# Optimization experiments

Measured on AMD Instinct MI355X. Metric: run time of the kernel, lower is better.

## Reference

```python
import jax, jax.numpy as jnp
import numpy as np

EPS = 1e-5

def _mlp(x, W1, b1, W2, b2):
    h = jax.nn.gelu(x @ W1 + b1, approximate=False)
    return h @ W2 + b2

def _ln(x, g, b):
    m = jnp.mean(x, axis=-1, keepdims=True)
    v = jnp.mean((x - m) ** 2, axis=-1, keepdims=True)
    return (x - m) * jax.lax.rsqrt(v + EPS) * g + b

def setup_inputs() -> dict:
    key = jax.random.key(0)
    B, N, D = 4, 256, 128
    ks = jax.random.split(key, 32)
    s = 0.02
    inp = {
        "node_h": jax.random.normal(ks[0], (B, N, D), jnp.float32),
        "pair_h": jax.random.normal(ks[1], (B, N, N, D), jnp.float32),
        "node_mask": jax.random.randint(ks[2], (B, N), 0, 2, jnp.int32),
        "edge_mask": jax.random.randint(ks[3], (B, N, N), 0, 2, jnp.int32),
        # node_from_pair MLP: 3D -> 2D -> D
        "nfp_W1": jax.random.normal(ks[4], (3 * D, 2 * D), jnp.float32) * s,
        "nfp_b1": jnp.zeros((2 * D,), jnp.float32),
        "nfp_W2": jax.random.normal(ks[5], (2 * D, D), jnp.float32) * s,
        "nfp_b2": jnp.zeros((D,), jnp.float32),
        # pair_from_node MLP: 5D -> 2D -> D
        "pfn_W1": jax.random.normal(ks[6], (5 * D, 2 * D), jnp.float32) * s,
        "pfn_b1": jnp.zeros((2 * D,), jnp.float32),
        "pfn_W2": jax.random.normal(ks[7], (2 * D, D), jnp.float32) * s,
        "pfn_b2": jnp.zeros((D,), jnp.float32),
        # node_ff: D -> 4D -> D
        "nff_W1": jax.random.normal(ks[8], (D, 4 * D), jnp.float32) * s,
        "nff_b1": jnp.zeros((4 * D,), jnp.float32),
        "nff_W2": jax.random.normal(ks[9], (4 * D, D), jnp.float32) * s,
        "nff_b2": jnp.zeros((D,), jnp.float32),
        # pair_ff: D -> 4D -> D
        "pff_W1": jax.random.normal(ks[10], (D, 4 * D), jnp.float32) * s,
        "pff_b1": jnp.zeros((4 * D,), jnp.float32),
        "pff_W2": jax.random.normal(ks[11], (4 * D, D), jnp.float32) * s,
        "pff_b2": jnp.zeros((D,), jnp.float32),
        # gates: 2D -> D, sigmoid
        "og_W": jax.random.normal(ks[12], (2 * D, D), jnp.float32) * s,
        "og_b": jnp.zeros((D,), jnp.float32),
        "ig_W": jax.random.normal(ks[13], (2 * D, D), jnp.float32) * s,
        "ig_b": jnp.zeros((D,), jnp.float32),
        # LayerNorms
        "nn1_g": jnp.ones((D,), jnp.float32), "nn1_b": jnp.zeros((D,), jnp.float32),
        "nn2_g": jnp.ones((D,), jnp.float32), "nn2_b": jnp.zeros((D,), jnp.float32),
        "pn1_g": jnp.ones((D,), jnp.float32), "pn1_b": jnp.zeros((D,), jnp.float32),
        "pn2_g": jnp.ones((D,), jnp.float32), "pn2_b": jnp.zeros((D,), jnp.float32),
    }
    return inp

def reference(node_h, pair_h, node_mask, edge_mask,
              nfp_W1, nfp_b1, nfp_W2, nfp_b2,
              pfn_W1, pfn_b1, pfn_W2, pfn_b2,
              nff_W1, nff_b1, nff_W2, nff_b2,
              pff_W1, pff_b1, pff_W2, pff_b2,
              og_W, og_b, ig_W, ig_b,
              nn1_g, nn1_b, nn2_g, nn2_b,
              pn1_g, pn1_b, pn2_g, pn2_b):
    vp = edge_mask.astype(jnp.float32)                       # [B,N,N]
    pair_m = pair_h * vp[..., None]                          # masked pairs
    out_deg = jnp.clip(vp.sum(axis=2), 1.0)[..., None]       # [B,N,1]
    in_deg = jnp.clip(vp.sum(axis=1), 1.0)[..., None]        # [B,N,1]
    out_ctx_raw = pair_m.sum(axis=2) / out_deg               # [B,N,D]
    in_ctx_raw = pair_m.sum(axis=1) / in_deg                 # [B,N,D]
    out_g = jax.nn.sigmoid(jnp.concatenate([node_h, out_ctx_raw], -1) @ og_W + og_b)
    in_g = jax.nn.sigmoid(jnp.concatenate([node_h, in_ctx_raw], -1) @ ig_W + ig_b)
    node_upd = _mlp(jnp.concatenate([node_h, out_g * out_ctx_raw, in_g * in_ctx_raw], -1),
                    nfp_W1, nfp_b1, nfp_W2, nfp_b2)
    node_h = _ln(node_h + node_upd, nn1_g, nn1_b)
    node_h = _ln(node_h + _mlp(node_h, nff_W1, nff_b1, nff_W2, nff_b2), nn2_g, nn2_b)
    node_h = node_h * node_mask.astype(jnp.float32)[..., None]

    B, N, D = node_h.shape
    hi = jnp.broadcast_to(node_h[:, :, None, :], (B, N, N, D))
    hj = jnp.broadcast_to(node_h[:, None, :, :], (B, N, N, D))
    feat = jnp.concatenate([pair_h, hi, hj, hi - hj, hi * hj], -1)  # [B,N,N,5D]
    pair_upd = _mlp(feat, pfn_W1, pfn_b1, pfn_W2, pfn_b2)
    pair_h = _ln(pair_h + pair_upd, pn1_g, pn1_b)
    pair_h = _ln(pair_h + _mlp(pair_h, pff_W1, pff_b1, pff_W2, pff_b2), pn2_g, pn2_b)
    pair_h = pair_h * vp[..., None]
    return (node_h, pair_h)
```

## Files before the change

kernel.cpp:

```cpp
#include <hip/hip_runtime.h>
#include <hip/hip_bf16.h>

#define DI __device__ __forceinline__

typedef float f32x4 __attribute__((ext_vector_type(4)));
typedef float f32x2 __attribute__((ext_vector_type(2)));
typedef short s16x8 __attribute__((ext_vector_type(8)));
typedef short s16x4 __attribute__((ext_vector_type(4)));
typedef unsigned u32x2 __attribute__((ext_vector_type(2)));
typedef unsigned u32x4 __attribute__((ext_vector_type(4)));

DI short f2bf(float x) {
  union { float f; unsigned u; } v; v.f = x;
  unsigned r = v.u + 0x7fffu + ((v.u >> 16) & 1u);
  return (short)(r >> 16);
}

DI float bf2f(short x) {
  union { unsigned u; float f; } v;
  v.u = ((unsigned)(unsigned short)x) << 16;
  return v.f;
}

DI unsigned cvt_pk(float lo, float hi) {
  unsigned r;
  asm("v_cvt_pk_bf16_f32 %0, %1, %2" : "=v"(r) : "v"(lo), "v"(hi));
  return r;
}

DI s16x8 pack8(f32x4 a, f32x4 b) {
  union { u32x4 u; s16x8 s; } r;
  r.u[0] = cvt_pk(a[0], a[1]); r.u[1] = cvt_pk(a[2], a[3]);
  r.u[2] = cvt_pk(b[0], b[1]); r.u[3] = cvt_pk(b[2], b[3]);
  return r.s;
}

DI float gelu_f(float x) {
  const float e = __expf(-x * fmaf(x * x, 0.0713548162f, 1.5957691216f));
  return __fdividef(x, 1.f + e);
}

__global__ __launch_bounds__(256) void prep_ctx_kernel(
    const float* __restrict__ pair_h, const int* __restrict__ edge_mask,
    const float* __restrict__ pfnW1, const float* __restrict__ pfnW2,
    const float* __restrict__ pffW1, const float* __restrict__ pffW2,
    short* __restrict__ W1c, float* __restrict__ Wu, float* __restrict__ Whjv,
    short* __restrict__ W2T, short* __restrict__ W1Tp,
    short* __restrict__ W2Tp, float* __restrict__ out_ctx,
    float* __restrict__ in_ctx) {
  __shared__ float sacc[2][128];
  __shared__ float sdeg[2];
  const int t = threadIdx.x;
  if (blockIdx.x >= 2048) {
    int idx = (blockIdx.x - 2048) * 256 + t;
    if (idx < 65536) {
      int n = idx / 256, k = idx % 256;
      float v = (k < 128) ? pfnW1[k * 256 + n] : pfnW1[(384 + k) * 256 + n];
      W1c[idx] = f2bf(v);
      return;
    }
    idx -= 65536;
    if (idx < 32768) {
      int k = idx / 256, n = idx % 256;
      Wu[idx] = pfnW1[(128 + k) * 256 + n] + pfnW1[(384 + k) * 256 + n];
      return;
    }
    idx -= 32768;
    if (idx < 32768) {
      int k = idx / 256, n = idx % 256;
      Whjv[idx] = pfnW1[(256 + k) * 256 + n] - pfnW1[(384 + k) * 256 + n];
      return;
    }
    idx -= 32768;
    if (idx < 32768) {
      int n = idx / 256, k = idx % 256;
      W2T[idx] = f2bf(pfnW2[k * 128 + n]);
      return;
    }
    idx -= 32768;
    if (idx < 65536) {
      int n = idx / 128, k = idx % 128;
      W1Tp[idx] = f2bf(pffW1[k * 512 + n]);
      return;
    }
    idx -= 65536;
    if (idx < 65536) {
      int n = idx / 512, k = idx % 512;
      W2Tp[idx] = f2bf(pffW2[k * 128 + n]);
    }
    return;
  }
  const int wg = blockIdx.x;
  const int half = t >> 7, d = t & 127;
  const bool outmode = wg < 1024;
  const int w2 = outmode ? wg : wg - 1024;
  const int b = w2 >> 8, x = w2 & 255;
  float acc = 0.f, deg = 0.f;
#pragma unroll 8
  for (int y0 = 0; y0 < 256; y0 += 2) {
    const int y = y0 + half;
    int row;
    if (outmode) row = (b * 256 + x) * 256 + y;
    else row = (b * 256 + y) * 256 + x;
    const float m = (float)edge_mask[row];
    const float v = pair_h[(long)row * 128 + d];
    acc = fmaf(m, v, acc);
    deg += m;
  }
  sacc[half][d] = acc;
  if (d == 0) sdeg[half] = deg;
  __syncthreads();
  if (t < 128) {
    float tot = sacc[0][d] + sacc[1][d];
    float dg = fmaxf(sdeg[0] + sdeg[1], 1.f);
    float* dst = outmode ? out_ctx : in_ctx;
    dst[(b * 256 + x) * 128 + d] = tot / dg;
  }
}

__global__ __launch_bounds__(256) void node_kernel(
    const float* __restrict__ node_h, const float* __restrict__ out_ctx,
    const float* __restrict__ in_ctx, const int* __restrict__ node_mask,
    const float* __restrict__ ogW, const float* __restrict__ ogb,
    const float* __restrict__ igW, const float* __restrict__ igb,
    const float* __restrict__ nW1, const float* __restrict__ nb1,
    const float* __restrict__ nW2, const float* __restrict__ nb2,
    const float* __restrict__ fW1, const float* __restrict__ fb1,
    const float* __restrict__ fW2, const float* __restrict__ fb2,
    const float* __restrict__ g1, const float* __restrict__ be1,
    const float* __restrict__ g2, const float* __restrict__ be2,
    const float* __restrict__ Wu, const float* __restrict__ ub1,
    const float* __restrict__ Whjv, float* __restrict__ out_node,
    short* __restrict__ node_bf, short* __restrict__ u_bf,
    short* __restrict__ hjv_bf) {
  __shared__ float sh[4][896];
  __shared__ float fin[4][128];
  const int t = threadIdx.x;
  const int wv = t >> 6, lane = t & 63;
  float* const xn = sh[wv];
  float* const xo = sh[wv] + 128;
  float* const xi = sh[wv] + 256;
  float* const hh = sh[wv] + 384;
  const int row = blockIdx.x * 4 + wv;

#pragma unroll
  for (int c = 0; c < 2; ++c) {
    const int col = lane + 64 * c;
    xn[col] = node_h[row * 128 + col];
    xo[col] = out_ctx[row * 128 + col];
    xi[col] = in_ctx[row * 128 + col];
  }

  {
    float ao[2], ai[2];
#pragma unroll
    for (int c = 0; c < 2; ++c) {
      const int col = lane + 64 * c;
      ao[c] = ogb[col];
      ai[c] = igb[col];
    }
#pragma unroll 4
    for (int k = 0; k < 256; ++k) {
      float xov, xiv;
      if (k < 128) { xov = xiv = xn[k]; }
      else { xov = xo[k - 128]; xiv = xi[k - 128]; }
#pragma unroll
      for (int c = 0; c < 2; ++c) {
        const int col = lane + 64 * c;
        ao[c] += xov * ogW[k * 128 + col];
        ai[c] += xiv * igW[k * 128 + col];
      }
    }
#pragma unroll
    for (int c = 0; c < 2; ++c) {
      const int col = lane + 64 * c;
      const float go = 1.f / (1.f + __expf(-ao[c]));
      const float gi = 1.f / (1.f + __expf(-ai[c]));
      xo[col] *= go;
      xi[col] *= gi;
    }
  }

  {
    float a1[4];
#pragma unroll
    for (int c = 0; c < 4; ++c) a1[c] = nb1[lane + 64 * c];
#pragma unroll 4
    for (int k = 0; k < 384; ++k) {
      const float* src = (k < 128) ? xn : (k < 256) ? xo : xi;
      const float x = src[k & 127];
#pragma unroll
      for (int c = 0; c < 4; ++c) a1[c] += x * nW1[k * 256 + lane + 64 * c];
    }
#pragma unroll
    for (int c = 0; c < 4; ++c) hh[lane + 64 * c] = gelu_f(a1[c]);
  }
  {
    float a2[2];
#pragma unroll
    for (int c = 0; c < 2; ++c) a2[c] = nb2[lane + 64 * c];
#pragma unroll 4
    for (int k = 0; k < 256; ++k) {
      const float h = hh[k];
#pragma unroll
      for (int c = 0; c < 2; ++c) a2[c] += h * nW2[k * 128 + lane + 64 * c];
    }
    float v0 = xn[lane] + a2[0];
    float v1 = xn[lane + 64] + a2[1];
    float s = v0 + v1, ss = v0 * v0 + v1 * v1;
#pragma unroll
    for (int off = 1; off < 64; off <<= 1) {
      s += __shfl_xor(s, off, 64);
      ss += __shfl_xor(ss, off, 64);
    }
    const float m = s * (1.f / 128.f);
    const float var = ss * (1.f / 128.f) - m * m;
    const float rs = rsqrtf(var + 1e-5f);
    xn[lane] = (v0 - m) * rs * g1[lane] + be1[lane];
    xn[lane + 64] = (v1 - m) * rs * g1[lane + 64] + be1[lane + 64];
  }

  {
    float af[8];
#pragma unroll
    for (int c = 0; c < 8; ++c) af[c] = fb1[lane + 64 * c];
#pragma unroll 4
    for (int k = 0; k < 128; ++k) {
      const float x = xn[k];
#pragma unroll
      for (int c = 0; c < 8; ++c) af[c] += x * fW1[k * 512 + lane + 64 * c];
    }
#pragma unroll
    for (int c = 0; c < 8; ++c) hh[lane + 64 * c] = gelu_f(af[c]);
  }
  {
    float a2[2];
#pragma unroll
    for (int c = 0; c < 2; ++c) a2[c] = fb2[lane + 64 * c];
#pragma unroll 4
    for (int k = 0; k < 512; ++k) {
      const float h = hh[k];
#pragma unroll
      for (int c = 0; c < 2; ++c) a2[c] += h * fW2[k * 128 + lane + 64 * c];
    }
    float v0 = xn[lane] + a2[0];
    float v1 = xn[lane + 64] + a2[1];
    float s = v0 + v1, ss = v0 * v0 + v1 * v1;
#pragma unroll
    for (int off = 1; off < 64; off <<= 1) {
      s += __shfl_xor(s, off, 64);
      ss += __shfl_xor(ss, off, 64);
    }
    const float m = s * (1.f / 128.f);
    const float var = ss * (1.f / 128.f) - m * m;
    const float rs = rsqrtf(var + 1e-5f);
    const float msk = (float)node_mask[row];
    const float o0 = ((v0 - m) * rs * g2[lane] + be2[lane]) * msk;
    const float o1 = ((v1 - m) * rs * g2[lane + 64] + be2[lane + 64]) * msk;
    out_node[row * 128 + lane] = o0;
    out_node[row * 128 + lane + 64] = o1;
    node_bf[row * 128 + lane] = f2bf(o0);
    node_bf[row * 128 + lane + 64] = f2bf(o1);
    fin[wv][lane] = o0;
    fin[wv][lane + 64] = o1;
  }
  __syncthreads();
  {
    float uacc[4], hacc[4];
    const float bb = ub1[t];
#pragma unroll
    for (int r = 0; r < 4; ++r) { uacc[r] = bb; hacc[r] = 0.f; }
#pragma unroll 4
    for (int k = 0; k < 128; ++k) {
      const float wu = Wu[k * 256 + t];
      const float wh = Whjv[k * 256 + t];
#pragma unroll
      for (int r = 0; r < 4; ++r) {
        uacc[r] += fin[r][k] * wu;
        hacc[r] += fin[r][k] * wh;
      }
    }
#pragma unroll
    for (int r = 0; r < 4; ++r) {
      u_bf[(blockIdx.x * 4 + r) * 256 + t] = f2bf(uacc[r]);
      hjv_bf[(blockIdx.x * 4 + r) * 256 + t] = f2bf(hacc[r]);
    }
  }
}

__global__ __launch_bounds__(512, 4) void pair_kernel(
    const float* __restrict__ pair_h, const short* __restrict__ node_bf,
    const int* __restrict__ edge_mask, const short* __restrict__ W1c,
    const short* __restrict__ W2T, const short* __restrict__ W1Tp,
    const short* __restrict__ W2Tp, const short* __restrict__ u_bf,
    const short* __restrict__ hjv_bf, const float* __restrict__ b2,
    const float* __restrict__ b1p, const float* __restrict__ b2p,
    const float* __restrict__ g1, const float* __restrict__ be1,
    const float* __restrict__ g2, const float* __restrict__ be2,
    float* __restrict__ out_pair) {
  constexpr int OFF_A = 0, OFF_H1 = 0, OFF_Y = 0, OFF_H2 = 33792,
                OFF_SCR = 67584;
  constexpr int PA = 528, PY = 272;
  __shared__ __align__(16) char smem[69632];

  const int t = threadIdx.x;
  const int wg = blockIdx.x;
  const int b = wg >> 10, rem = wg & 1023;
  const int i = rem >> 2, j0 = (rem & 3) << 6;
  const int bi = (b << 8) + i;
  const long rowbase = (long)bi * 256 + j0;

  const int lane = t & 63, wv = t >> 6;
  const int lr = lane & 15, lq = lane >> 4;
  const int jb = (wv >> 2) * 32, nb2 = (wv & 3) * 32;

  {
    const int r = t >> 3, oc = t & 7, c0 = oc * 16;
    const float* prow = pair_h + (rowbase + r) * 128 + c0;
    const short* hjrow = node_bf + (b * 256 + j0 + r) * 128 + c0;
    const short* hirow = node_bf + (b * 256 + i) * 128 + c0;
    char* arow = smem + OFF_A + r * PA;
#pragma unroll
    for (int h = 0; h < 2; ++h) {
      f32x4 p0 = *(const f32x4*)(prow + h * 8);
      f32x4 p1 = *(const f32x4*)(prow + h * 8 + 4);
      s16x8 hj = *(const s16x8*)(hjrow + h * 8);
      s16x8 hi = *(const s16x8*)(hirow + h * 8);
      *(s16x8*)(arow + c0 * 2 + h * 16) = pack8(p0, p1);
      union { u32x4 u; s16x8 s; } pd;
#pragma unroll
      for (int e = 0; e < 4; ++e)
        pd.u[e] = cvt_pk(bf2f(hi[2 * e]) * bf2f(hj[2 * e]),
                         bf2f(hi[2 * e + 1]) * bf2f(hj[2 * e + 1]));
      *(s16x8*)(arow + 256 + c0 * 2 + h * 16) = pd.s;
    }
  }
  __syncthreads();

  f32x4 acc1[4][2];
#pragma unroll
  for (int jt = 0; jt < 4; ++jt)
#pragma unroll
    for (int nt = 0; nt < 2; ++nt) acc1[jt][nt] = {0.f, 0.f, 0.f, 0.f};
  {
    const int nb = wv * 32;
    const short* wp0 = W1c + (nb + lr) * 256 + lq * 8;
    const short* wp1 = W1c + (nb + 16 + lr) * 256 + lq * 8;
    s16x8 w0p[4], w1p[4];
#pragma unroll
    for (int pf = 0; pf < 4; ++pf) {
      w0p[pf] = *(const s16x8*)(wp0 + pf * 32);
      w1p[pf] = *(const s16x8*)(wp1 + pf * 32);
    }
    s16x8 dc[2][4];
#pragma unroll
    for (int pf = 0; pf < 2; ++pf)
#pragma unroll
      for (int jt = 0; jt < 4; ++jt)
        dc[pf][jt] = *(const s16x8*)(smem + OFF_A + (jt * 16 + lr) * PA +
                                     pf * 64 + lq * 16);
#pragma unroll
    for (int ks = 0; ks < 8; ++ks) {
      const int cur = ks & 1;
      s16x8 w0 = w0p[ks & 3], w1 = w1p[ks & 3];
      if (ks < 4) {
        w0p[ks & 3] = *(const s16x8*)(wp0 + (ks + 4) * 32);
        w1p[ks & 3] = *(const s16x8*)(wp1 + (ks + 4) * 32);
      }
      s16x8 d[4];
#pragma unroll
      for (int jt = 0; jt < 4; ++jt) d[jt] = dc[cur][jt];
      if (ks < 6) {
#pragma unroll
        for (int jt = 0; jt < 4; ++jt)
          dc[cur][jt] = *(const s16x8*)(smem + OFF_A + (jt * 16 + lr) * PA +
                                        (ks + 2) * 64 + lq * 16);
      }
#pragma unroll
      for (int jt = 0; jt < 4; ++jt) {
        acc1[jt][0] = __builtin_amdgcn_mfma_f32_16x16x32_bf16(w0, d[jt], acc1[jt][0], 0, 0, 0);
        acc1[jt][1] = __builtin_amdgcn_mfma_f32_16x16x32_bf16(w1, d[jt], acc1[jt][1], 0, 0, 0);
      }
    }
  }
  s16x4 uv0 = *(const s16x4*)(u_bf + bi * 256 + wv * 32 + lq * 4);
  s16x4 uv1 = *(const s16x4*)(u_bf + bi * 256 + wv * 32 + 16 + lq * 4);
  const short* q2p0 = W2T + (nb2 + lr) * 256 + lq * 8;
  const short* q2p1 = W2T + (nb2 + 16 + lr) * 256 + lq * 8;
  s16x8 q2w0[4], q2w1[4];
  q2w0[0] = *(const s16x8*)q2p0;
  q2w1[0] = *(const s16x8*)q2p1;
  q2w0[1] = *(const s16x8*)(q2p0 + 32);
  q2w1[1] = *(const s16x8*)(q2p1 + 32);
  __syncthreads();
  {
    const int nb = wv * 32;
#pragma unroll
    for (int nt = 0; nt < 2; ++nt) {
      const int n0 = nb + nt * 16 + lq * 4;
      const s16x4 uv = nt ? uv1 : uv0;
      f32x4 uu;
#pragma unroll
      for (int v = 0; v < 4; ++v) uu[v] = bf2f(uv[v]);
#pragma unroll
      for (int jt = 0; jt < 4; ++jt) {
        const int j = jt * 16 + lr;
        s16x4 hv = *(const s16x4*)(hjv_bf + (b * 256 + j0 + j) * 256 + n0);
        float pre[4];
#pragma unroll
        for (int v = 0; v < 4; ++v)
          pre[v] = acc1[jt][nt][v] + uu[v] + bf2f(hv[v]);
        u32x2 pk = {cvt_pk(gelu_f(pre[0]), gelu_f(pre[1])),
                    cvt_pk(gelu_f(pre[2]), gelu_f(pre[3]))};
        *(u32x2*)(smem + OFF_H1 + j * PA + n0 * 2) = pk;
      }
    }
  }
  __syncthreads();

  f32x4 x1v[2][2];
  {
    q2w0[2] = *(const s16x8*)(q2p0 + 64);
    q2w1[2] = *(const s16x8*)(q2p1 + 64);
    q2w0[3] = *(const s16x8*)(q2p0 + 96);
    q2w1[3] = *(const s16x8*)(q2p1 + 96);
    f32x4 pr[2][2];
#pragma unroll
    for (int nt = 0; nt < 2; ++nt)
#pragma unroll
      for (int jt = 0; jt < 2; ++jt)
        pr[jt][nt] = *(const f32x4*)(pair_h + (rowbase + jb + jt * 16 + lr) * 128 +
                                     nb2 + nt * 16 + lq * 4);
    s16x8 dc[2][2];
#pragma unroll
    for (int pf = 0; pf < 2; ++pf)
#pragma unroll
      for (int jt = 0; jt < 2; ++jt)
        dc[pf][jt] = *(const s16x8*)(smem + OFF_H1 + (jb + jt * 16 + lr) * PA +
                                     pf * 64 + lq * 16);
    f32x4 acc2[2][2];
#pragma unroll
    for (int jt = 0; jt < 2; ++jt)
#pragma unroll
      for (int nt = 0; nt < 2; ++nt) acc2[jt][nt] = {0.f, 0.f, 0.f, 0.f};
#pragma unroll
    for (int ks = 0; ks < 8; ++ks) {
      const int cur = ks & 1;
      s16x8 w0 = q2w0[ks & 3], w1 = q2w1[ks & 3];
      if (ks < 4) {
        q2w0[ks & 3] = *(const s16x8*)(q2p0 + (ks + 4) * 32);
        q2w1[ks & 3] = *(const s16x8*)(q2p1 + (ks + 4) * 32);
      }
      s16x8 d[2];
#pragma unroll
      for (int jt = 0; jt < 2; ++jt) d[jt] = dc[cur][jt];
      if (ks < 6) {
#pragma unroll
        for (int jt = 0; jt < 2; ++jt)
          dc[cur][jt] = *(const s16x8*)(smem + OFF_H1 + (jb + jt * 16 + lr) * PA +
                                        (ks + 2) * 64 + lq * 16);
      }
#pragma unroll
      for (int jt = 0; jt < 2; ++jt) {
        acc2[jt][0] = __builtin_amdgcn_mfma_f32_16x16x32_bf16(w0, d[jt], acc2[jt][0], 0, 0, 0);
        acc2[jt][1] = __builtin_amdgcn_mfma_f32_16x16x32_bf16(w1, d[jt], acc2[jt][1], 0, 0, 0);
      }
    }
#pragma unroll
    for (int nt = 0; nt < 2; ++nt) {
      const int n0 = nb2 + nt * 16 + lq * 4;
      f32x4 bv = *(const f32x4*)(b2 + n0);
#pragma unroll
      for (int jt = 0; jt < 2; ++jt)
        x1v[jt][nt] = acc2[jt][nt] + bv + pr[jt][nt];
    }
  }
  {
    float s[2], ss[2];
#pragma unroll
    for (int jt = 0; jt < 2; ++jt) {
      s[jt] = 0.f; ss[jt] = 0.f;
#pragma unroll
      for (int nt = 0; nt < 2; ++nt)
#pragma unroll
        for (int v = 0; v < 4; ++v) {
          const float x = x1v[jt][nt][v];
          s[jt] += x; ss[jt] += x * x;
        }
      s[jt] += __shfl_xor(s[jt], 16, 64);
      ss[jt] += __shfl_xor(ss[jt], 16, 64);
      s[jt] += __shfl_xor(s[jt], 32, 64);
      ss[jt] += __shfl_xor(ss[jt], 32, 64);
    }
    if (lq == 0) {
#pragma unroll
      for (int jt = 0; jt < 2; ++jt) {
        const int j = jb + jt * 16 + lr;
        f32x2 p = {s[jt], ss[jt]};
        *(f32x2*)(smem + OFF_SCR + j * 32 + (wv & 3) * 8) = p;
      }
    }
    __syncthreads();
    float lnm[2], lnr[2];
#pragma unroll
    for (int jt = 0; jt < 2; ++jt) {
      const int j = jb + jt * 16 + lr;
      f32x4 pA = *(const f32x4*)(smem + OFF_SCR + j * 32);
      f32x4 pB = *(const f32x4*)(smem + OFF_SCR + j * 32 + 16);
      const float S = pA[0] + pA[2] + pB[0] + pB[2];
      const float SS = pA[1] + pA[3] + pB[1] + pB[3];
      const float m = S * (1.f / 128.f);
      const float var = SS * (1.f / 128.f) - m * m;
      lnm[jt] = m;
      lnr[jt] = rsqrtf(var + 1e-5f);
    }
#pragma unroll
    for (int nt = 0; nt < 2; ++nt) {
      const int n0 = nb2 + nt * 16 + lq * 4;
      f32x4 gv = *(const f32x4*)(g1 + n0);
      f32x4 bv = *(const f32x4*)(be1 + n0);
#pragma unroll
      for (int jt = 0; jt < 2; ++jt) {
        const int j = jb + jt * 16 + lr;
        float y[4];
#pragma unroll
        for (int v = 0; v < 4; ++v)
          y[v] = (x1v[jt][nt][v] - lnm[jt]) * lnr[jt] * gv[v] + bv[v];
        u32x2 pk = {cvt_pk(y[0], y[1]), cvt_pk(y[2], y[3])};
        *(u32x2*)(smem + OFF_Y + j * PY + n0 * 2) = pk;
      }
    }
  }
  const short* g3p0a = W1Tp + (wv * 32 + lr) * 128 + lq * 8;
  const short* g3p1a = W1Tp + (wv * 32 + 16 + lr) * 128 + lq * 8;
  s16x8 g3w0[4], g3w1[4];
  g3w0[0] = *(const s16x8*)g3p0a;
  g3w1[0] = *(const s16x8*)g3p1a;
  g3w0[1] = *(const s16x8*)(g3p0a + 32);
  g3w1[1] = *(const s16x8*)(g3p1a + 32);
  const int em0 = edge_mask[rowbase + jb + lr];
  const int em1 = edge_mask[rowbase + jb + 16 + lr];
  __syncthreads();

  f32x4 acc4[2][2];
#pragma unroll
  for (int jt = 0; jt < 2; ++jt)
#pragma unroll
    for (int nt = 0; nt < 2; ++nt) acc4[jt][nt] = {0.f, 0.f, 0.f, 0.f};

#pragma unroll
  for (int p = 0; p < 2; ++p) {
    f32x4 acc3[4][2];
#pragma unroll
    for (int jt = 0; jt < 4; ++jt)
#pragma unroll
      for (int nt = 0; nt < 2; ++nt) acc3[jt][nt] = {0.f, 0.f, 0.f, 0.f};
    {
      const int nb3 = p * 256 + wv * 32;
      const short* wp0 = W1Tp + (nb3 + lr) * 128 + lq * 8;
      const short* wp1 = W1Tp + (nb3 + 16 + lr) * 128 + lq * 8;
      if (p == 0) {
        g3w0[2] = *(const s16x8*)(wp0 + 64);
        g3w1[2] = *(const s16x8*)(wp1 + 64);
        g3w0[3] = *(const s16x8*)(wp0 + 96);
        g3w1[3] = *(const s16x8*)(wp1 + 96);
      } else {
#pragma unroll
        for (int pf = 0; pf < 4; ++pf) {
          g3w0[pf] = *(const s16x8*)(wp0 + pf * 32);
          g3w1[pf] = *(const s16x8*)(wp1 + pf * 32);
        }
      }
#pragma unroll
      for (int ks = 0; ks < 4; ++ks) {
        s16x8 d[4];
#pragma unroll
        for (int jt = 0; jt < 4; ++jt)
          d[jt] = *(const s16x8*)(smem + OFF_Y + (jt * 16 + lr) * PY +
                                  ks * 64 + lq * 16);
#pragma unroll
        for (int jt = 0; jt < 4; ++jt) {
          acc3[jt][0] = __builtin_amdgcn_mfma_f32_16x16x32_bf16(g3w0[ks], d[jt], acc3[jt][0], 0, 0, 0);
          acc3[jt][1] = __builtin_amdgcn_mfma_f32_16x16x32_bf16(g3w1[ks], d[jt], acc3[jt][1], 0, 0, 0);
        }
      }
    }
    const short* qp0 = W2Tp + (nb2 + lr) * 512 + p * 256 + lq * 8;
    const short* qp1 = W2Tp + (nb2 + 16 + lr) * 512 + p * 256 + lq * 8;
    s16x8 q4w0[4], q4w1[4];
    q4w0[0] = *(const s16x8*)qp0;
    q4w1[0] = *(const s16x8*)qp1;
    q4w0[1] = *(const s16x8*)(qp0 + 32);
    q4w1[1] = *(const s16x8*)(qp1 + 32);
    if (p == 1) __syncthreads();
    {
#pragma unroll
      for (int nt = 0; nt < 2; ++nt) {
        const int n0l = wv * 32 + nt * 16 + lq * 4;
        f32x4 bv = *(const f32x4*)(b1p + p * 256 + n0l);
#pragma unroll
        for (int jt = 0; jt < 4; ++jt) {
          const int j = jt * 16 + lr;
          u32x2 pk = {cvt_pk(gelu_f(acc3[jt][nt][0] + bv[0]),
                             gelu_f(acc3[jt][nt][1] + bv[1])),
                      cvt_pk(gelu_f(acc3[jt][nt][2] + bv[2]),
                             gelu_f(acc3[jt][nt][3] + bv[3]))};
          *(u32x2*)(smem + OFF_H2 + j * PA + n0l * 2) = pk;
        }
      }
    }
    __syncthreads();
    {
      q4w0[2] = *(const s16x8*)(qp0 + 64);
      q4w1[2] = *(const s16x8*)(qp1 + 64);
      q4w0[3] = *(const s16x8*)(qp0 + 96);
      q4w1[3] = *(const s16x8*)(qp1 + 96);
      s16x8 dc[2][2];
#pragma unroll
      for (int pf = 0; pf < 2; ++pf)
#pragma unroll
        for (int jt = 0; jt < 2; ++jt)
          dc[pf][jt] = *(const s16x8*)(smem + OFF_H2 + (jb + jt * 16 + lr) * PA +
                                       pf * 64 + lq * 16);
#pragma unroll
      for (int ks = 0; ks < 8; ++ks) {
        const int cur = ks & 1;
        s16x8 w0 = q4w0[ks & 3], w1 = q4w1[ks & 3];
        if (ks < 4) {
          q4w0[ks & 3] = *(const s16x8*)(qp0 + (ks + 4) * 32);
          q4w1[ks & 3] = *(const s16x8*)(qp1 + (ks + 4) * 32);
        }
        s16x8 d[2];
#pragma unroll
        for (int jt = 0; jt < 2; ++jt) d[jt] = dc[cur][jt];
        if (ks < 6) {
#pragma unroll
          for (int jt = 0; jt < 2; ++jt)
            dc[cur][jt] = *(const s16x8*)(smem + OFF_H2 + (jb + jt * 16 + lr) * PA +
                                          (ks + 2) * 64 + lq * 16);
        }
#pragma unroll
        for (int jt = 0; jt < 2; ++jt) {
          acc4[jt][0] = __builtin_amdgcn_mfma_f32_16x16x32_bf16(w0, d[jt], acc4[jt][0], 0, 0, 0);
          acc4[jt][1] = __builtin_amdgcn_mfma_f32_16x16x32_bf16(w1, d[jt], acc4[jt][1], 0, 0, 0);
        }
      }
    }
  }

  f32x4 x2v[2][2];
#pragma unroll
  for (int nt = 0; nt < 2; ++nt) {
    const int n0 = nb2 + nt * 16 + lq * 4;
    f32x4 bv = *(const f32x4*)(b2p + n0);
#pragma unroll
    for (int jt = 0; jt < 2; ++jt) {
      const int j = jb + jt * 16 + lr;
      s16x4 yv = *(const s16x4*)(smem + OFF_Y + j * PY + n0 * 2);
      f32x4 yr;
#pragma unroll
      for (int v = 0; v < 4; ++v) yr[v] = bf2f(yv[v]);
      x2v[jt][nt] = acc4[jt][nt] + bv + yr;
    }
  }
  {
    float s[2], ss[2];
#pragma unroll
    for (int jt = 0; jt < 2; ++jt) {
      s[jt] = 0.f; ss[jt] = 0.f;
#pragma unroll
      for (int nt = 0; nt < 2; ++nt)
#pragma unroll
        for (int v = 0; v < 4; ++v) {
          const float x = x2v[jt][nt][v];
          s[jt] += x; ss[jt] += x * x;
        }
      s[jt] += __shfl_xor(s[jt], 16, 64);
      ss[jt] += __shfl_xor(ss[jt], 16, 64);
      s[jt] += __shfl_xor(s[jt], 32, 64);
      ss[jt] += __shfl_xor(ss[jt], 32, 64);
    }
    if (lq == 0) {
#pragma unroll
      for (int jt = 0; jt < 2; ++jt) {
        const int j = jb + jt * 16 + lr;
        f32x2 p = {s[jt], ss[jt]};
        *(f32x2*)(smem + OFF_SCR + j * 32 + (wv & 3) * 8) = p;
      }
    }
    __syncthreads();
    float lnm[2], lnr[2], vp[2];
#pragma unroll
    for (int jt = 0; jt < 2; ++jt) {
      const int j = jb + jt * 16 + lr;
      f32x4 pA = *(const f32x4*)(smem + OFF_SCR + j * 32);
      f32x4 pB = *(const f32x4*)(smem + OFF_SCR + j * 32 + 16);
      const float S = pA[0] + pA[2] + pB[0] + pB[2];
      const float SS = pA[1] + pA[3] + pB[1] + pB[3];
      const float m = S * (1.f / 128.f);
      const float var = SS * (1.f / 128.f) - m * m;
      lnm[jt] = m;
      lnr[jt] = rsqrtf(var + 1e-5f);
      vp[jt] = (float)(jt ? em1 : em0);
    }
#pragma unroll
    for (int nt = 0; nt < 2; ++nt) {
      const int n0 = nb2 + nt * 16 + lq * 4;
      f32x4 gv = *(const f32x4*)(g2 + n0);
      f32x4 bv = *(const f32x4*)(be2 + n0);
#pragma unroll
      for (int jt = 0; jt < 2; ++jt) {
        const int j = jb + jt * 16 + lr;
        f32x4 o;
#pragma unroll
        for (int v = 0; v < 4; ++v)
          o[v] = ((x2v[jt][nt][v] - lnm[jt]) * lnr[jt] * gv[v] + bv[v]) * vp[jt];
        *(f32x4*)(out_pair + (rowbase + j) * 128 + n0) = o;
      }
    }
  }
}

extern "C" void kernel_launch(void* const* d_in, const int* in_sizes, int n_in,
                              void* d_out, int out_size, void* d_ws,
                              size_t ws_size, hipStream_t stream) {
  const float* node_h = (const float*)d_in[0];
  const float* pair_h = (const float*)d_in[1];
  const int* node_mask = (const int*)d_in[2];
  const int* edge_mask = (const int*)d_in[3];
  const float* nfp_W1 = (const float*)d_in[4];
  const float* nfp_b1 = (const float*)d_in[5];
  const float* nfp_W2 = (const float*)d_in[6];
  const float* nfp_b2 = (const float*)d_in[7];
  const float* pfn_W1 = (const float*)d_in[8];
  const float* pfn_b1 = (const float*)d_in[9];
  const float* pfn_W2 = (const float*)d_in[10];
  const float* pfn_b2 = (const float*)d_in[11];
  const float* nff_W1 = (const float*)d_in[12];
  const float* nff_b1 = (const float*)d_in[13];
  const float* nff_W2 = (const float*)d_in[14];
  const float* nff_b2 = (const float*)d_in[15];
  const float* pff_W1 = (const float*)d_in[16];
  const float* pff_b1 = (const float*)d_in[17];
  const float* pff_W2 = (const float*)d_in[18];
  const float* pff_b2 = (const float*)d_in[19];
  const float* og_W = (const float*)d_in[20];
  const float* og_b = (const float*)d_in[21];
  const float* ig_W = (const float*)d_in[22];
  const float* ig_b = (const float*)d_in[23];
  const float* nn1_g = (const float*)d_in[24];
  const float* nn1_b = (const float*)d_in[25];
  const float* nn2_g = (const float*)d_in[26];
  const float* nn2_b = (const float*)d_in[27];
  const float* pn1_g = (const float*)d_in[28];
  const float* pn1_b = (const float*)d_in[29];
  const float* pn2_g = (const float*)d_in[30];
  const float* pn2_b = (const float*)d_in[31];

  char* ws = (char*)d_ws;
  short* W1c = (short*)(ws);
  short* W2T = (short*)(ws + 131072);
  short* W1Tp = (short*)(ws + 196608);
  short* W2Tp = (short*)(ws + 327680);
  float* Wu = (float*)(ws + 458752);
  float* Whjv = (float*)(ws + 589824);
  float* out_ctx = (float*)(ws + 720896);
  float* in_ctx = (float*)(ws + 1245184);
  short* node_bf = (short*)(ws + 1769472);
  short* u_bf = (short*)(ws + 2031616);
  short* hjv_bf = (short*)(ws + 2555904);

  float* out_node = (float*)d_out;
  float* out_pair = (float*)d_out + 131072;

  prep_ctx_kernel<<<3200, 256, 0, stream>>>(
      pair_h, edge_mask, pfn_W1, pfn_W2, pff_W1, pff_W2, W1c, Wu, Whjv, W2T,
      W1Tp, W2Tp, out_ctx, in_ctx);
  node_kernel<<<256, 256, 0, stream>>>(
      node_h, out_ctx, in_ctx, node_mask, og_W, og_b, ig_W, ig_b, nfp_W1,
      nfp_b1, nfp_W2, nfp_b2, nff_W1, nff_b1, nff_W2, nff_b2, nn1_g, nn1_b,
      nn2_g, nn2_b, Wu, pfn_b1, Whjv, out_node, node_bf, u_bf, hjv_bf);
  pair_kernel<<<4096, 512, 0, stream>>>(
      pair_h, node_bf, edge_mask, W1c, W2T, W1Tp, W2Tp, u_bf, hjv_bf, pfn_b2,
      pff_b1, pff_b2, pn1_g, pn1_b, pn2_g, pn2_b, out_pair);
}
```

Measured before the change: 568.2 us.

## Split in-context reduction into coalesced partial sums plus separate reduce kernel

Replaces the strided column-wise reduction over pair_h for the incoming context with blocks that read contiguous rows in 16-row chunks and emit bf16 partial sums and partial degrees. A new small kernel sums the partials per column and divides by degree. This targets uncoalesced, widely strided global reads, at the cost of an extra launch, scratch traffic, and bf16 rounding of partial sums; scratch may fall back to the tail of the output buffer.

```diff
diff --git a/kernel.cpp b/kernel.cpp
--- a/kernel.cpp
+++ b/kernel.cpp
@@ -47,12 +47,12 @@
     short* __restrict__ W1c, float* __restrict__ Wu, float* __restrict__ Whjv,
     short* __restrict__ W2T, short* __restrict__ W1Tp,
     short* __restrict__ W2Tp, float* __restrict__ out_ctx,
-    float* __restrict__ in_ctx) {
+    short* __restrict__ pin, float* __restrict__ pdeg) {
   __shared__ float sacc[2][128];
   __shared__ float sdeg[2];
   const int t = threadIdx.x;
-  if (blockIdx.x >= 2048) {
-    int idx = (blockIdx.x - 2048) * 256 + t;
+  if (blockIdx.x >= 1088) {
+    int idx = (blockIdx.x - 1088) * 256 + t;
     if (idx < 65536) {
       int n = idx / 256, k = idx % 256;
       float v = (k < 128) ? pfnW1[k * 256 + n] : pfnW1[(384 + k) * 256 + n];
@@ -90,20 +90,41 @@
     }
     return;
   }
+  if (blockIdx.x >= 1024) {
+    const int bx = blockIdx.x - 1024;
+    const int b = bx >> 4, c = bx & 15;
+    const int i0 = c * 16;
+    const int d4 = (t & 31) * 4;
+    const int jrow = t >> 5;
+    for (int jo = 0; jo < 32; ++jo) {
+      const int j = jo * 8 + jrow;
+      f32x4 acc = {0.f, 0.f, 0.f, 0.f};
+      float dg = 0.f;
+#pragma unroll
+      for (int i = 0; i < 16; ++i) {
+        const long row = (long)(b * 256 + i0 + i) * 256 + j;
+        const float m = (float)edge_mask[row];
+        f32x4 v = *(const f32x4*)(pair_h + row * 128 + d4);
+#pragma unroll
+        for (int e = 0; e < 4; ++e) acc[e] = fmaf(m, v[e], acc[e]);
+        dg += m;
+      }
+      u32x2 pk = {cvt_pk(acc[0], acc[1]), cvt_pk(acc[2], acc[3])};
+      *(u32x2*)(pin + ((long)bx * 256 + j) * 128 + d4) = pk;
+      if ((t & 31) == 0) pdeg[bx * 256 + j] = dg;
+    }
+    return;
+  }
   const int wg = blockIdx.x;
   const int half = t >> 7, d = t & 127;
-  const bool outmode = wg < 1024;
-  const int w2 = outmode ? wg : wg - 1024;
-  const int b = w2 >> 8, x = w2 & 255;
+  const int b = wg >> 8, x = wg & 255;
   float acc = 0.f, deg = 0.f;
 #pragma unroll 8
   for (int y0 = 0; y0 < 256; y0 += 2) {
     const int y = y0 + half;
-    int row;
-    if (outmode) row = (b * 256 + x) * 256 + y;
-    else row = (b * 256 + y) * 256 + x;
+    const long row = (long)(b * 256 + x) * 256 + y;
     const float m = (float)edge_mask[row];
-    const float v = pair_h[(long)row * 128 + d];
+    const float v = pair_h[row * 128 + d];
     acc = fmaf(m, v, acc);
     deg += m;
   }
@@ -113,9 +134,25 @@
   if (t < 128) {
     float tot = sacc[0][d] + sacc[1][d];
     float dg = fmaxf(sdeg[0] + sdeg[1], 1.f);
-    float* dst = outmode ? out_ctx : in_ctx;
-    dst[(b * 256 + x) * 128 + d] = tot / dg;
-  }
+    out_ctx[(b * 256 + x) * 128 + d] = tot / dg;
+  }
+}
+
+__global__ __launch_bounds__(256) void inred_kernel(
+    const short* __restrict__ pin, const float* __restrict__ pdeg,
+    float* __restrict__ in_ctx) {
+  const int tid = blockIdx.x * 256 + threadIdx.x;
+  const int d = tid & 127;
+  const int j = (tid >> 7) & 255;
+  const int b = tid >> 15;
+  float s = 0.f, dg = 0.f;
+#pragma unroll
+  for (int c = 0; c < 16; ++c) {
+    const int bx = b * 16 + c;
+    s += bf2f(pin[((long)bx * 256 + j) * 128 + d]);
+    dg += pdeg[bx * 256 + j];
+  }
+  in_ctx[(b * 256 + j) * 128 + d] = s / fmaxf(dg, 1.f);
 }
 
 __global__ __launch_bounds__(256) void node_kernel(
@@ -770,12 +807,25 @@
   short* u_bf = (short*)(ws + 2031616);
   short* hjv_bf = (short*)(ws + 2555904);
 
+  const size_t scratch_need = 3080192ull + 4194304ull + 65536ull;
+  short* pin;
+  float* pdeg;
+  if (ws_size >= scratch_need) {
+    pin = (short*)(ws + 3080192);
+    pdeg = (float*)(ws + 3080192 + 4194304);
+  } else {
+    char* tail = (char*)d_out + (size_t)out_size * 4 - 4259840ull;
+    pin = (short*)tail;
+    pdeg = (float*)(tail + 4194304);
+  }
+
   float* out_node = (float*)d_out;
   float* out_pair = (float*)d_out + 131072;
 
-  prep_ctx_kernel<<<3200, 256, 0, stream>>>(
+  prep_ctx_kernel<<<2240, 256, 0, stream>>>(
       pair_h, edge_mask, pfn_W1, pfn_W2, pff_W1, pff_W2, W1c, Wu, Whjv, W2T,
-      W1Tp, W2Tp, out_ctx, in_ctx);
+      W1Tp, W2Tp, out_ctx, pin, pdeg);
+  inred_kernel<<<512, 256, 0, stream>>>(pin, pdeg, in_ctx);
   node_kernel<<<256, 256, 0, stream>>>(
       node_h, out_ctx, in_ctx, node_mask, og_W, og_b, ig_W, ig_b, nfp_W1,
       nfp_b1, nfp_W2, nfp_b2, nff_W1, nff_b1, nff_W2, nff_b2, nn1_g, nn1_b,
```

Result: slower. 583.6 us (+2.7%).
